# Kernel optimization log

Measured on AMD Instinct MI355X. Metric: run time of the kernel, lower is better.

Reference implementation:

```python
import jax, jax.numpy as jnp
import numpy as np
from jax import lax

B, N, H, W, C = 8, 1024, 256, 256, 256
HID = 512
RATES = (1, 3, 9, 9, 3, 1)


def setup_inputs() -> dict:
    key = jax.random.key(0)
    ks = jax.random.split(key, 16)
    # vertices are (row, col) float coordinates inside the feature map
    vertices = jax.random.uniform(ks[0], (B, N, 2), jnp.float32) * jnp.array([H - 1, W - 1], jnp.float32)
    features = jax.random.normal(ks[1], (B, H, W, C), jnp.float32)
    inp = {"vertices": vertices, "features": features}
    # Conv1D stack params (haiku Conv1D: kernel [K, Cin, Cout], bias [Cout])
    cin = C
    for i in range(6):
        inp[f"w{i}"] = jax.random.normal(ks[2 + 2 * i], (3, cin, HID), jnp.float32) * 0.05
        inp[f"b{i}"] = jax.random.normal(ks[3 + 2 * i], (HID,), jnp.float32) * 0.05
        cin = HID
    # offset head: Conv1D(2, 1, with_bias=False); original zero-init, randomized here
    inp["w_off"] = jax.random.normal(ks[14], (1, HID, 2), jnp.float32) * 0.05
    return inp


def _conv1d(x, w, b, rate):
    # x: [B, N, Cin], w: [K, Cin, Cout] -> SAME-padded dilated conv over vertex axis
    y = lax.conv_general_dilated(x, w, window_strides=(1,), padding="SAME",
                                 rhs_dilation=(rate,),
                                 dimension_numbers=("NWC", "WIO", "NWC"))
    return y if b is None else y + b


def _sample_at_vertices(vertices, features):
    # bilinear interpolation, zero outside (map_coordinates order=1 mode='constant')
    Bb, Hh, Ww, Cc = features.shape
    y, x = vertices[..., 0], vertices[..., 1]  # [B, N]
    y0f, x0f = jnp.floor(y), jnp.floor(x)
    wy1, wx1 = y - y0f, x - x0f
    wy0, wx0 = 1.0 - wy1, 1.0 - wx1
    y0, x0 = y0f.astype(jnp.int32), x0f.astype(jnp.int32)
    flat = features.reshape(Bb, Hh * Ww, Cc)

    def gather(yi, xi, wgt):
        valid = (yi >= 0) & (yi < Hh) & (xi >= 0) & (xi < Ww)
        idx = jnp.clip(yi, 0, Hh - 1) * Ww + jnp.clip(xi, 0, Ww - 1)  # [B, N]
        vals = jnp.take_along_axis(flat, idx[..., None], axis=1)  # [B, N, C]
        return vals * (wgt * valid)[..., None]

    return (gather(y0, x0, wy0 * wx0) + gather(y0, x0 + 1, wy0 * wx1)
            + gather(y0 + 1, x0, wy1 * wx0) + gather(y0 + 1, x0 + 1, wy1 * wx1))


def reference(vertices, features, w0, b0, w1, b1, w2, b2, w3, b3, w4, b4, w5, b5, w_off):
    h = _sample_at_vertices(vertices, features)  # [B, N, C]
    ws = (w0, w1, w2, w3, w4, w5)
    bs = (b0, b1, b2, b3, b4, b5)
    for w, b, r in zip(ws, bs, RATES):
        h = jax.nn.relu(_conv1d(h, w, b, r))
    offsets = _conv1d(h, w_off, None, 1)  # [B, N, 2]
    return vertices + offsets
```

## Files before the change

kernel.cpp:

```cpp
#include <hip/hip_runtime.h>

#define BATCH 8
#define NPTS  1024
#define FH    256
#define FW    256
#define FC    256
#define HID   512
#define PADN  1056
#define HALO  16

typedef __attribute__((ext_vector_type(8))) short short8;
typedef __attribute__((ext_vector_type(16))) float f32x16;
typedef unsigned short ushort_t;
typedef unsigned int uint_t;

__device__ __forceinline__ ushort_t f2bf(float f) {
    uint_t u = __builtin_bit_cast(uint_t, f);
    u += 0x7fffu + ((u >> 16) & 1u);
    return (ushort_t)(u >> 16);
}
__device__ __forceinline__ float bf2f(ushort_t s) {
    uint_t u = ((uint_t)s) << 16;
    return __builtin_bit_cast(float, u);
}

#define GLOAD16(g, l)                                                     \
    __builtin_amdgcn_global_load_lds(                                     \
        (const __attribute__((address_space(1))) void*)(g),               \
        (__attribute__((address_space(3))) void*)(l), 16, 0, 0)

__device__ __forceinline__ short8 gread16(const short* p) {
    short8 r;
    asm volatile("global_load_dwordx4 %0, %1, off" : "=v"(r) : "v"(p));
    return r;
}

__global__ __launch_bounds__(256) void prep_kernel(
    const float* __restrict__ vertices, const float* __restrict__ features,
    const float* __restrict__ w0, const float* __restrict__ w1,
    const float* __restrict__ w2, const float* __restrict__ w3,
    const float* __restrict__ w4, const float* __restrict__ w5,
    ushort_t* __restrict__ wt0, ushort_t* __restrict__ wt1,
    ushort_t* __restrict__ wt2, ushort_t* __restrict__ wt3,
    ushort_t* __restrict__ wt4, ushort_t* __restrict__ wt5,
    ushort_t* __restrict__ XpA, ushort_t* __restrict__ XpB,
    ushort_t* __restrict__ XpC)
{
    __shared__ float tile[64][65];
    const int blk = blockIdx.x;
    const int tid = threadIdx.x;

    if (blk < 1280) {
        int i = blk * 256 + tid;
        if (i < 65536) {
            int b = i >> 13, rem = i & 8191;
            int strip = rem >> 12, off = rem & 4095;
            XpA[(size_t)b * (PADN * FC) + (strip ? (PADN - HALO) * FC : 0) + off] = 0;
        }
        int jB = i - 65536;
        if (jB >= 0 && jB < 262144) {
            ushort_t* T = (jB < 131072) ? XpB : XpC;
            int j = jB & 131071;
            int b = j >> 14, rem = j & 16383;
            int strip = rem >> 13, off = rem & 8191;
            T[(size_t)b * (PADN * HID) + (strip ? (PADN - HALO) * HID : 0) + off] = 0;
        }
        return;
    }

    if (blk < 2336) {
        int j = blk - 1280;
        const float* w; ushort_t* wt; int CIN, kk0, co0;
        if (j < 96) {
            w = w0; wt = wt0; CIN = FC;
            kk0 = (j % 12) * 64; co0 = (j / 12) * 64;
        } else {
            int j2 = j - 96;
            int layer = j2 / 192, jj = j2 % 192;
            const float* ws[5]  = {w1, w2, w3, w4, w5};
            ushort_t*   wts[5]  = {wt1, wt2, wt3, wt4, wt5};
            w = ws[layer]; wt = wts[layer]; CIN = HID;
            kk0 = (jj % 24) * 64; co0 = (jj / 24) * 64;
        }
        int tap = kk0 / CIN, ci0 = kk0 - tap * CIN;
        int SL  = (3 * CIN) >> 4;
#pragma unroll 4
        for (int it = 0; it < 16; ++it) {
            int r = it * 4 + (tid >> 6);
            tile[r][tid & 63] = w[((size_t)tap * CIN + ci0 + r) * HID + co0 + (tid & 63)];
        }
        __syncthreads();
        int gl  = tid >> 7;
        int r2  = tid & 127;
        int l   = r2 >> 1;
        int j0  = (r2 & 1) * 4;
        int gco = (co0 >> 5) + gl;
        int kb  = ((l >> 5) << 3);
        int cl  = gl * 32 + (l & 31);
#pragma unroll
        for (int si = 0; si < 4; ++si) {
            int s = (kk0 >> 4) + si;
            ushort4 v;
            v.x = f2bf(tile[si * 16 + kb + j0 + 0][cl]);
            v.y = f2bf(tile[si * 16 + kb + j0 + 1][cl]);
            v.z = f2bf(tile[si * 16 + kb + j0 + 2][cl]);
            v.w = f2bf(tile[si * 16 + kb + j0 + 3][cl]);
            *(ushort4*)(wt + ((((size_t)gco * SL) + s) << 9) + l * 8 + j0) = v;
        }
        return;
    }

    {
        int p = (blk - 2336) * 4 + (tid >> 6);
        int b = p >> 10;
        int n = p & 1023;
        int t = tid & 63;

        float y = vertices[2 * p + 0];
        float x = vertices[2 * p + 1];
        float y0f = floorf(y), x0f = floorf(x);
        float wy1 = y - y0f, wx1 = x - x0f;
        float wy0 = 1.f - wy1, wx0 = 1.f - wx1;
        int y0 = (int)y0f, x0 = (int)x0f;

        float4 acc = make_float4(0.f, 0.f, 0.f, 0.f);
        const float4* fbase = (const float4*)features + (size_t)b * FH * FW * (FC / 4);

#define CORNER(yi, xi, wgt) {                                                  \
        int yy = (yi), xx = (xi);                                              \
        float wv = ((yy >= 0) && (yy < FH) && (xx >= 0) && (xx < FW)) ? (wgt) : 0.f; \
        int yc = yy < 0 ? 0 : (yy > FH - 1 ? FH - 1 : yy);                     \
        int xc = xx < 0 ? 0 : (xx > FW - 1 ? FW - 1 : xx);                     \
        float4 v = fbase[((size_t)yc * FW + xc) * (FC / 4) + t];               \
        acc.x += v.x * wv; acc.y += v.y * wv; acc.z += v.z * wv; acc.w += v.w * wv; }

        CORNER(y0,     x0,     wy0 * wx0);
        CORNER(y0,     x0 + 1, wy0 * wx1);
        CORNER(y0 + 1, x0,     wy1 * wx0);
        CORNER(y0 + 1, x0 + 1, wy1 * wx1);
#undef CORNER

        ushort4 o;
        o.x = f2bf(acc.x); o.y = f2bf(acc.y); o.z = f2bf(acc.z); o.w = f2bf(acc.w);
        *(ushort4*)(XpA + ((size_t)b * PADN + HALO + n) * FC + 4 * t) = o;
    }
}

template <int CIN>
__global__ __launch_bounds__(256, 2) void conv_mfma(
    const ushort_t* __restrict__ Xp,
    const ushort_t* __restrict__ Wf,
    const float* __restrict__ bias,
    ushort_t* __restrict__ Yp,
    int rate)
{
    constexpr int NC  = CIN / 64;
    constexpr int SL3 = CIN / 16;
    constexpr int SL  = 3 * SL3;
    __shared__ short lds[3][10240];

    const int tid  = threadIdx.x;
    const int wid  = tid >> 6;
    const int lane = tid & 63;
    const int wm   = wid >> 1, wn = wid & 1;

    const int h  = blockIdx.x;
    const int bm = (h & 7) * 8 + (h >> 6);
    const int bn = (h >> 3) & 7;
    const int batch = bm >> 3;
    const int n0    = (bm & 7) * 128;
    const int co0   = bn * 64;

    const short* Xbase = (const short*)Xp + ((size_t)batch * PADN + n0) * CIN;
    const short* Wb = (const short*)Wf
                    + (((size_t)(bn * 2 + wn) * SL) << 9) + lane * 8;

    auto stageA = [&](int buf, int c) {
        const short* Ag = Xbase + c * 64;
        short* ldsA = &lds[buf][0];
#pragma unroll
        for (int it = 0; it < 5; ++it) {
            int slot = it * 256 + wid * 64 + lane;
            int row  = slot >> 3;
            int chnk = (slot & 7) ^ (row & 7);
            GLOAD16(Ag + (size_t)row * CIN + chnk * 8,
                    ldsA + (size_t)(it * 256 + wid * 64) * 8);
        }
    };
    auto loadB = [&](short8* dst, int c) {
#pragma unroll
        for (int t = 0; t < 3; ++t)
#pragma unroll
            for (int ks = 0; ks < 4; ++ks)
                dst[t * 4 + ks] = gread16(Wb + ((size_t)(t * SL3 + c * 4 + ks) << 9));
    };

    f32x16 acc[2];
    const int rowA0 = wm * 64 + (lane & 31);
    const int coB   = wn * 32 + (lane & 31);
    {
        float bv = bias[co0 + coB];
#pragma unroll
        for (int i = 0; i < 2; ++i)
#pragma unroll
            for (int r = 0; r < 16; ++r) acc[i][r] = bv;
    }

    short8 B0[12], B1[12];
    stageA(0, 0);
    __builtin_amdgcn_sched_barrier(0);
    loadB(B0, 0);
    __builtin_amdgcn_sched_barrier(0);
    stageA(1, 1);
    __builtin_amdgcn_sched_barrier(0);

    int cur = 0;
    auto kstep = [&](int c, short8* Bcur, short8* Bnxt) {
        if (c == NC - 1) asm volatile("s_waitcnt vmcnt(0)" ::: "memory");
        else             asm volatile("s_waitcnt vmcnt(5)" ::: "memory");
        __builtin_amdgcn_s_barrier();
        __builtin_amdgcn_sched_barrier(0);

        if (c + 1 < NC) loadB(Bnxt, c + 1);
        __builtin_amdgcn_sched_barrier(0);
        if (c + 2 < NC) {
            int nb = cur + 2; if (nb >= 3) nb -= 3;
            stageA(nb, c + 2);
        }
        __builtin_amdgcn_sched_barrier(0);

        const short* As = &lds[cur][0];
        __builtin_amdgcn_s_setprio(1);
#pragma unroll
        for (int t = 0; t < 3; ++t) {
            const int shift = 16 + (t - 1) * rate;
            short8 av[2][4];
#pragma unroll
            for (int ks = 0; ks < 4; ++ks) {
                int ch = ks * 2 + (lane >> 5);
#pragma unroll
                for (int i = 0; i < 2; ++i) {
                    int rr = rowA0 + i * 32 + shift;
                    av[i][ks] = *(const short8*)(As + rr * 64 + ((ch ^ (rr & 7)) << 3));
                }
            }
#pragma unroll
            for (int ks = 0; ks < 4; ++ks)
#pragma unroll
                for (int i = 0; i < 2; ++i)
                    acc[i] = __builtin_amdgcn_mfma_f32_32x32x16_bf16(
                        av[i][ks], Bcur[t * 4 + ks], acc[i], 0, 0, 0);
        }
        __builtin_amdgcn_s_setprio(0);
        cur += 1; if (cur >= 3) cur -= 3;
    };

    for (int c = 0; c < NC; c += 2) {
        kstep(c,     B0, B1);
        kstep(c + 1, B1, B0);
    }

    ushort_t* Yb = Yp + ((size_t)batch * PADN + HALO + n0) * HID + co0;
#pragma unroll
    for (int i = 0; i < 2; ++i) {
#pragma unroll
        for (int r = 0; r < 16; ++r) {
            int rrow = wm * 64 + i * 32 + (r & 3) + 8 * (r >> 2) + 4 * (lane >> 5);
            float v = acc[i][r];
            v = v > 0.f ? v : 0.f;
            Yb[(size_t)rrow * HID + coB] = f2bf(v);
        }
    }
}

__global__ __launch_bounds__(64) void head_kernel(
    const ushort_t* __restrict__ h, const float* __restrict__ w_off,
    const float* __restrict__ vertices, float* __restrict__ out)
{
    int p = blockIdx.x;
    int b = p >> 10, n = p & 1023;
    int t = threadIdx.x;
    const ushort_t* hr = h + ((size_t)b * PADN + HALO + n) * HID + t * 8;

    uint4 raw = *(const uint4*)hr;
    ushort_t hv[8];
    hv[0] = raw.x & 0xffff; hv[1] = raw.x >> 16;
    hv[2] = raw.y & 0xffff; hv[3] = raw.y >> 16;
    hv[4] = raw.z & 0xffff; hv[5] = raw.z >> 16;
    hv[6] = raw.w & 0xffff; hv[7] = raw.w >> 16;

    float s0 = 0.f, s1 = 0.f;
#pragma unroll
    for (int k = 0; k < 8; ++k) {
        float x = bf2f(hv[k]);
        s0 += x * w_off[(t * 8 + k) * 2 + 0];
        s1 += x * w_off[(t * 8 + k) * 2 + 1];
    }
#pragma unroll
    for (int off = 32; off >= 1; off >>= 1) {
        s0 += __shfl_down(s0, off);
        s1 += __shfl_down(s1, off);
    }
    if (t == 0) {
        out[2 * p + 0] = vertices[2 * p + 0] + s0;
        out[2 * p + 1] = vertices[2 * p + 1] + s1;
    }
}

extern "C" void kernel_launch(void* const* d_in, const int* in_sizes, int n_in,
                              void* d_out, int out_size, void* d_ws, size_t ws_size,
                              hipStream_t stream)
{
    (void)in_sizes; (void)n_in; (void)out_size; (void)ws_size;

    const float* vertices = (const float*)d_in[0];
    const float* features = (const float*)d_in[1];
    const float* w[6]  = {(const float*)d_in[2], (const float*)d_in[4],
                          (const float*)d_in[6], (const float*)d_in[8],
                          (const float*)d_in[10], (const float*)d_in[12]};
    const float* bb[6] = {(const float*)d_in[3], (const float*)d_in[5],
                          (const float*)d_in[7], (const float*)d_in[9],
                          (const float*)d_in[11], (const float*)d_in[13]};
    const float* w_off = (const float*)d_in[14];
    float* out = (float*)d_out;

    char* p = (char*)d_ws;
    ushort_t* wt[6];
    wt[0] = (ushort_t*)p; p += (size_t)HID * (3 * FC) * 2;
    for (int i = 1; i < 6; ++i) { wt[i] = (ushort_t*)p; p += (size_t)HID * (3 * HID) * 2; }
    ushort_t* XpA = (ushort_t*)p; p += (size_t)BATCH * PADN * FC  * 2;
    ushort_t* XpB = (ushort_t*)p; p += (size_t)BATCH * PADN * HID * 2;
    ushort_t* XpC = (ushort_t*)p;

    prep_kernel<<<4384, 256, 0, stream>>>(
        vertices, features, w[0], w[1], w[2], w[3], w[4], w[5],
        wt[0], wt[1], wt[2], wt[3], wt[4], wt[5], XpA, XpB, XpC);

    static const int rates[6] = {1, 3, 9, 9, 3, 1};
    conv_mfma<FC><<<512, 256, 0, stream>>>(XpA, wt[0], bb[0], XpB, rates[0]);
    ushort_t* src = XpB;
    ushort_t* dst = XpC;
    for (int i = 1; i < 6; ++i) {
        conv_mfma<HID><<<512, 256, 0, stream>>>(src, wt[i], bb[i], dst, rates[i]);
        ushort_t* tmp = src; src = dst; dst = tmp;
    }

    head_kernel<<<BATCH * NPTS, 64, 0, stream>>>(src, w_off, vertices, out);
}
```

Before: 121.9 us.

## Split K across wave pairs in conv kernel with LDS reduction, 512-thread blocks

Each conv block now runs 8 waves instead of 4. Each pair of waves splits the 64-channel K chunk in half, and the partial accumulators are summed through LDS before the ReLU and bf16 store. The A-tile pipeline drops from triple to double buffering with a different wait and barrier placement, and the weight register footprint per wave is halved. The aim is more waves per CU to hide latency. The cost is an extra LDS reduction at the end and a shallower prefetch depth.

```diff
diff --git a/kernel.cpp b/kernel.cpp
--- a/kernel.cpp
+++ b/kernel.cpp
@@ -147,7 +147,7 @@
 }
 
 template <int CIN>
-__global__ __launch_bounds__(256, 2) void conv_mfma(
+__global__ __launch_bounds__(512, 4) void conv_mfma(
     const ushort_t* __restrict__ Xp,
     const ushort_t* __restrict__ Wf,
     const float* __restrict__ bias,
@@ -157,12 +157,14 @@
     constexpr int NC  = CIN / 64;
     constexpr int SL3 = CIN / 16;
     constexpr int SL  = 3 * SL3;
-    __shared__ short lds[3][10240];
+    __shared__ short lds[2][10240];
 
     const int tid  = threadIdx.x;
     const int wid  = tid >> 6;
     const int lane = tid & 63;
-    const int wm   = wid >> 1, wn = wid & 1;
+    const int wm   = wid >> 2;
+    const int wn   = (wid >> 1) & 1;
+    const int wk   = wid & 1;
 
     const int h  = blockIdx.x;
     const int bm = (h & 7) * 8 + (h >> 6);
@@ -179,54 +181,57 @@
         const short* Ag = Xbase + c * 64;
         short* ldsA = &lds[buf][0];
 #pragma unroll
-        for (int it = 0; it < 5; ++it) {
-            int slot = it * 256 + wid * 64 + lane;
+        for (int it = 0; it < 2; ++it) {
+            int slot = it * 512 + wid * 64 + lane;
             int row  = slot >> 3;
             int chnk = (slot & 7) ^ (row & 7);
             GLOAD16(Ag + (size_t)row * CIN + chnk * 8,
-                    ldsA + (size_t)(it * 256 + wid * 64) * 8);
+                    ldsA + (size_t)(it * 512 + wid * 64) * 8);
+        }
+        if (wid < 4) {
+            int slot = 1024 + wid * 64 + lane;
+            int row  = slot >> 3;
+            int chnk = (slot & 7) ^ (row & 7);
+            GLOAD16(Ag + (size_t)row * CIN + chnk * 8,
+                    ldsA + (size_t)(1024 + wid * 64) * 8);
         }
     };
     auto loadB = [&](short8* dst, int c) {
 #pragma unroll
         for (int t = 0; t < 3; ++t)
 #pragma unroll
-            for (int ks = 0; ks < 4; ++ks)
-                dst[t * 4 + ks] = gread16(Wb + ((size_t)(t * SL3 + c * 4 + ks) << 9));
+            for (int ksh = 0; ksh < 2; ++ksh)
+                dst[t * 2 + ksh] =
+                    gread16(Wb + ((size_t)(t * SL3 + c * 4 + wk * 2 + ksh) << 9));
     };
 
     f32x16 acc[2];
     const int rowA0 = wm * 64 + (lane & 31);
     const int coB   = wn * 32 + (lane & 31);
     {
-        float bv = bias[co0 + coB];
+        float bv = (wk == 0) ? bias[co0 + coB] : 0.f;
 #pragma unroll
         for (int i = 0; i < 2; ++i)
 #pragma unroll
             for (int r = 0; r < 16; ++r) acc[i][r] = bv;
     }
 
-    short8 B0[12], B1[12];
+    short8 B0[6], B1[6];
     stageA(0, 0);
     __builtin_amdgcn_sched_barrier(0);
     loadB(B0, 0);
     __builtin_amdgcn_sched_barrier(0);
-    stageA(1, 1);
+    asm volatile("s_waitcnt vmcnt(6)" ::: "memory");
+    __builtin_amdgcn_s_barrier();
     __builtin_amdgcn_sched_barrier(0);
 
     int cur = 0;
     auto kstep = [&](int c, short8* Bcur, short8* Bnxt) {
-        if (c == NC - 1) asm volatile("s_waitcnt vmcnt(0)" ::: "memory");
-        else             asm volatile("s_waitcnt vmcnt(5)" ::: "memory");
-        __builtin_amdgcn_s_barrier();
+        if (c + 1 < NC) stageA(cur ^ 1, c + 1);
         __builtin_amdgcn_sched_barrier(0);
 
-        if (c + 1 < NC) loadB(Bnxt, c + 1);
-        __builtin_amdgcn_sched_barrier(0);
-        if (c + 2 < NC) {
-            int nb = cur + 2; if (nb >= 3) nb -= 3;
-            stageA(nb, c + 2);
-        }
+        if (c + 1 < NC) asm volatile("s_waitcnt vmcnt(2)" ::: "memory");
+        else            asm volatile("s_waitcnt vmcnt(0)" ::: "memory");
         __builtin_amdgcn_sched_barrier(0);
 
         const short* As = &lds[cur][0];
@@ -234,25 +239,28 @@
 #pragma unroll
         for (int t = 0; t < 3; ++t) {
             const int shift = 16 + (t - 1) * rate;
-            short8 av[2][4];
-#pragma unroll
-            for (int ks = 0; ks < 4; ++ks) {
-                int ch = ks * 2 + (lane >> 5);
+#pragma unroll
+            for (int ksh = 0; ksh < 2; ++ksh) {
+                int ch = (wk * 2 + ksh) * 2 + (lane >> 5);
 #pragma unroll
                 for (int i = 0; i < 2; ++i) {
                     int rr = rowA0 + i * 32 + shift;
-                    av[i][ks] = *(const short8*)(As + rr * 64 + ((ch ^ (rr & 7)) << 3));
+                    short8 av = *(const short8*)(As + rr * 64 + ((ch ^ (rr & 7)) << 3));
+                    acc[i] = __builtin_amdgcn_mfma_f32_32x32x16_bf16(
+                        av, Bcur[t * 2 + ksh], acc[i], 0, 0, 0);
                 }
             }
-#pragma unroll
-            for (int ks = 0; ks < 4; ++ks)
-#pragma unroll
-                for (int i = 0; i < 2; ++i)
-                    acc[i] = __builtin_amdgcn_mfma_f32_32x32x16_bf16(
-                        av[i][ks], Bcur[t * 4 + ks], acc[i], 0, 0, 0);
         }
         __builtin_amdgcn_s_setprio(0);
-        cur += 1; if (cur >= 3) cur -= 3;
+        __builtin_amdgcn_sched_barrier(0);
+
+        if (c + 1 < NC) {
+            loadB(Bnxt, c + 1);
+            __builtin_amdgcn_sched_barrier(0);
+            asm volatile("s_waitcnt vmcnt(6)" ::: "memory");
+        }
+        __builtin_amdgcn_s_barrier();
+        cur ^= 1;
     };
 
     for (int c = 0; c < NC; c += 2) {
@@ -260,15 +268,27 @@
         kstep(c + 1, B1, B0);
     }
 
-    ushort_t* Yb = Yp + ((size_t)batch * PADN + HALO + n0) * HID + co0;
-#pragma unroll
-    for (int i = 0; i < 2; ++i) {
-#pragma unroll
-        for (int r = 0; r < 16; ++r) {
-            int rrow = wm * 64 + i * 32 + (r & 3) + 8 * (r >> 2) + 4 * (lane >> 5);
-            float v = acc[i][r];
-            v = v > 0.f ? v : 0.f;
-            Yb[(size_t)rrow * HID + coB] = f2bf(v);
+    float* pf = (float*)&lds[0][0];
+    const int pair = wm * 2 + wn;
+    if (wk == 1) {
+#pragma unroll
+        for (int i = 0; i < 2; ++i)
+#pragma unroll
+            for (int r = 0; r < 16; ++r)
+                pf[pair * 2048 + (i * 16 + r) * 64 + lane] = acc[i][r];
+    }
+    __syncthreads();
+    if (wk == 0) {
+        ushort_t* Yb = Yp + ((size_t)batch * PADN + HALO + n0) * HID + co0;
+#pragma unroll
+        for (int i = 0; i < 2; ++i) {
+#pragma unroll
+            for (int r = 0; r < 16; ++r) {
+                int rrow = wm * 64 + i * 32 + (r & 3) + 8 * (r >> 2) + 4 * (lane >> 5);
+                float v = acc[i][r] + pf[pair * 2048 + (i * 16 + r) * 64 + lane];
+                v = v > 0.f ? v : 0.f;
+                Yb[(size_t)rrow * HID + coB] = f2bf(v);
+            }
         }
     }
 }
@@ -337,11 +357,11 @@
         wt[0], wt[1], wt[2], wt[3], wt[4], wt[5], XpA, XpB, XpC);
 
     static const int rates[6] = {1, 3, 9, 9, 3, 1};
-    conv_mfma<FC><<<512, 256, 0, stream>>>(XpA, wt[0], bb[0], XpB, rates[0]);
+    conv_mfma<FC><<<512, 512, 0, stream>>>(XpA, wt[0], bb[0], XpB, rates[0]);
     ushort_t* src = XpB;
     ushort_t* dst = XpC;
     for (int i = 1; i < 6; ++i) {
-        conv_mfma<HID><<<512, 256, 0, stream>>>(src, wt[i], bb[i], dst, rates[i]);
+        conv_mfma<HID><<<512, 512, 0, stream>>>(src, wt[i], bb[i], dst, rates[i]);
         ushort_t* tmp = src; src = dst; dst = tmp;
     }
 
```

Result: no change. 121.3 us (-0.5%).
